# Performance work log

Hardware: AMD Instinct MI355X
Metric: run time of the kernel (lower is better)

## Reference

```python
import jax, jax.numpy as jnp
import numpy as np


def setup_inputs() -> dict:
    key = jax.random.key(0)
    k1, k2, k3, k4 = jax.random.split(key, 4)
    N, E, D_IN, D_OUT = 100000, 1600000, 128, 128
    x = jax.random.normal(k1, (N, D_IN), dtype=jnp.float32)
    # nn.Linear weight has shape [out_channels, in_channels]
    weight = jax.random.normal(k2, (D_OUT, D_IN), dtype=jnp.float32) * (1.0 / np.sqrt(D_IN))
    # COO sparse A_hat: row 0 = dst (i), row 1 = src (j)
    edge_index = jax.random.randint(k3, (2, E), 0, N, dtype=jnp.int64)
    edge_vals = jax.random.uniform(k4, (E,), dtype=jnp.float32)
    return {
        "x": x,
        "weight": weight,
        "edge_index": edge_index,
        "edge_vals": edge_vals,
        "num_nodes": N,
    }


def reference(x, weight, edge_index, edge_vals, num_nodes):
    # H = x @ W^T  (nn.Linear without bias)
    h = jnp.einsum("ni,oi->no", x, weight)  # [N, out]
    dst = edge_index[0]
    src = edge_index[1]
    # sparse A_hat @ H: out[i] = sum over edges (i<-j) of a_ij * h[j]
    msgs = edge_vals[:, None] * h[src]  # [E, out]
    out = jax.ops.segment_sum(msgs, dst, num_segments=num_nodes)
    return out
```

## Files before the change

### kernel.cpp

```cpp
#include <hip/hip_runtime.h>

#define D 128
#define SCAN_BLK 1024
#define BM 64
#define BM2 128
#define KC 32
#define BSH 6
#define BNODES 64

using short8 = __attribute__((ext_vector_type(8))) short;
using floatx4 = __attribute__((ext_vector_type(4))) float;

__device__ __forceinline__ unsigned int f2bf(unsigned int b) {
    return (b + 0x7fffu + ((b >> 16) & 1u)) >> 16;
}

__global__ void transpose_w_kernel(const float* __restrict__ w, float* __restrict__ wt) {
    int t = blockIdx.x * 256 + threadIdx.x;
    if (t < D * D) {
        int o = t >> 7;
        int k = t & 127;
        wt[k * D + o] = w[t];
    }
}

__global__ void prep_wbfs_kernel(const float* __restrict__ w, unsigned short* __restrict__ wbfs) {
    int t = blockIdx.x * 256 + threadIdx.x;
    if (t < D * D) {
        int n = t >> 7, k = t & 127;
        wbfs[n * 128 + (k ^ ((n & 7) << 3))] = (unsigned short)f2bf(__float_as_uint(w[t]));
    }
}

__global__ __launch_bounds__(256) void x_to_bf16_kernel(const float* __restrict__ x,
                                                        unsigned int* __restrict__ xbf,
                                                        long long nvec) {
    long long i = (long long)blockIdx.x * 256 + threadIdx.x;
    long long stride = (long long)gridDim.x * 256;
    for (; i < nvec; i += stride) {
        float4 v = ((const float4*)x)[i];
        unsigned int b0 = f2bf(__float_as_uint(v.x)), b1 = f2bf(__float_as_uint(v.y));
        unsigned int b2 = f2bf(__float_as_uint(v.z)), b3 = f2bf(__float_as_uint(v.w));
        ((uint2*)xbf)[i] = make_uint2(b0 | (b1 << 16), b2 | (b3 << 16));
    }
}

__global__ __launch_bounds__(512) void bhist_kernel(const int* __restrict__ ei, int* bhist,
                                                    int E, int NB) {
    __shared__ int h[2048];
    int tid = threadIdx.x;
    for (int i = tid; i < NB; i += 512) h[i] = 0;
    __syncthreads();
    for (long long e = (long long)blockIdx.x * 512 + tid; e < E; e += (long long)gridDim.x * 512)
        atomicAdd(&h[((unsigned)ei[e]) >> BSH], 1);
    __syncthreads();
    for (int i = tid; i < NB; i += 512)
        if (h[i]) atomicAdd(&bhist[i], h[i]);
}

__global__ __launch_bounds__(SCAN_BLK) void scan_blocks_kernel(const int* __restrict__ deg,
                                                               int* inscan, int* blksum, int n) {
    __shared__ int s[SCAN_BLK];
    int gid = blockIdx.x * SCAN_BLK + threadIdx.x;
    int v = (gid < n) ? deg[gid] : 0;
    s[threadIdx.x] = v;
    __syncthreads();
    for (int d = 1; d < SCAN_BLK; d <<= 1) {
        int t = (threadIdx.x >= d) ? s[threadIdx.x - d] : 0;
        __syncthreads();
        s[threadIdx.x] += t;
        __syncthreads();
    }
    if (gid < n) inscan[gid] = s[threadIdx.x];
    if (threadIdx.x == SCAN_BLK - 1) blksum[blockIdx.x] = s[SCAN_BLK - 1];
}

__global__ __launch_bounds__(128) void scan_sums_kernel(const int* __restrict__ blksum,
                                                        int* blkoff, int nblk) {
    __shared__ int s[128];
    int v = (threadIdx.x < nblk) ? blksum[threadIdx.x] : 0;
    s[threadIdx.x] = v;
    __syncthreads();
    for (int d = 1; d < 128; d <<= 1) {
        int t = (threadIdx.x >= d) ? s[threadIdx.x - d] : 0;
        __syncthreads();
        s[threadIdx.x] += t;
        __syncthreads();
    }
    if (threadIdx.x < nblk) blkoff[threadIdx.x] = s[threadIdx.x] - v;
}

__global__ void bucket_finalize_kernel(const int* __restrict__ bhist,
                                       const int* __restrict__ binscan,
                                       const int* __restrict__ bblkoff,
                                       int* bbase, int* bcursor, int* off,
                                       int NB, int N, int E) {
    int g = blockIdx.x * 256 + threadIdx.x;
    if (g < NB) {
        int o = bblkoff[g >> 10] + binscan[g] - bhist[g];
        bbase[g] = o;
        bcursor[g] = o;
    }
    if (g == 0) { bbase[NB] = E; off[N] = E; }
}

__global__ __launch_bounds__(512) void binA_kernel(const int* __restrict__ ei,
                                                   const float* __restrict__ ev,
                                                   int* bcursor, int2* __restrict__ ebin,
                                                   int E, int NB) {
    __shared__ int hist[2048];
    __shared__ int base[2048];
    __shared__ int cnt2[2048];
    int tid = threadIdx.x;
    for (int i = tid; i < NB; i += 512) { hist[i] = 0; cnt2[i] = 0; }
    __syncthreads();
    int e0 = blockIdx.x * 8192;
#pragma unroll
    for (int i = 0; i < 16; ++i) {
        int e = e0 + i * 512 + tid;
        if (e < E) atomicAdd(&hist[((unsigned)ei[e]) >> BSH], 1);
    }
    __syncthreads();
    for (int i = tid; i < NB; i += 512)
        if (hist[i]) base[i] = atomicAdd(&bcursor[i], hist[i]);
    __syncthreads();
#pragma unroll
    for (int i = 0; i < 16; ++i) {
        int e = e0 + i * 512 + tid;
        if (e < E) {
            int dst = ei[e];
            int b = ((unsigned)dst) >> BSH;
            int pos = base[b] + atomicAdd(&cnt2[b], 1);
            ebin[pos] = make_int2(ei[E + e] | ((dst & (BNODES - 1)) << 26),
                                  __float_as_int(ev[e]));
        }
    }
}

__global__ __launch_bounds__(512) void binB2_kernel(const int* __restrict__ bbase,
                                                    const int2* __restrict__ ebin,
                                                    int* __restrict__ off,
                                                    int2* __restrict__ srt, int N) {
    __shared__ int degL[BNODES];
    __shared__ int cum[BNODES];
    __shared__ int cnt2[BNODES];
    int b = blockIdx.x;
    int tid = threadIdx.x;
    if (tid < BNODES) { degL[tid] = 0; cnt2[tid] = 0; }
    __syncthreads();
    int start = bbase[b], end = bbase[b + 1];
    for (int p = start + tid; p < end; p += 512)
        atomicAdd(&degL[((unsigned)ebin[p].x) >> 26], 1);
    __syncthreads();
    if (tid == 0) {
        int run = start;
#pragma unroll
        for (int i = 0; i < BNODES; ++i) { cum[i] = run; run += degL[i]; }
    }
    __syncthreads();
    int node0 = b << BSH;
    if (tid < BNODES && node0 + tid < N) off[node0 + tid] = cum[tid];
    for (int p = start + tid; p < end; p += 512) {
        int2 eb = ebin[p];
        int dl = ((unsigned)eb.x) >> 26;
        int pos = cum[dl] + atomicAdd(&cnt2[dl], 1);
        srt[pos] = make_int2(eb.x & 0x03FFFFFF, eb.y);
    }
}

__global__ void hist_rank_kernel(const int* __restrict__ ei, int* deg,
                                 unsigned short* __restrict__ rank, int E) {
    int e = blockIdx.x * 256 + threadIdx.x;
    if (e < E) rank[e] = (unsigned short)atomicAdd(&deg[ei[e]], 1);
}

__global__ void finalize_offsets_kernel(const int* __restrict__ deg,
                                        const int* __restrict__ inscan,
                                        const int* __restrict__ blkoff,
                                        int* off, int n, int E) {
    int gid = blockIdx.x * 256 + threadIdx.x;
    if (gid < n) off[gid] = blkoff[gid >> 10] + inscan[gid] - deg[gid];
    if (gid == 0) off[n] = E;
}

__global__ void edge_scatter2_kernel(const int* __restrict__ ei, const float* __restrict__ ev,
                                     const int* __restrict__ off,
                                     const unsigned short* __restrict__ rank,
                                     int2* __restrict__ srt, int E) {
    int e = blockIdx.x * 256 + threadIdx.x;
    if (e < E) {
        int dst = ei[e];
        int pos = off[dst] + (int)rank[e];
        srt[pos] = make_int2(ei[E + e], __float_as_int(ev[e]));
    }
}

template <bool AGGBF>
__global__ __launch_bounds__(256) void gather_bf16_kernel(const int* __restrict__ off,
                                                          const int2* __restrict__ srt,
                                                          const unsigned int* __restrict__ xbf,
                                                          float* __restrict__ out,
                                                          unsigned int* __restrict__ aggbf,
                                                          int N) {
    int lane = threadIdx.x & 63;
    int wid = blockIdx.x * 4 + (threadIdx.x >> 6);
    if (wid >= N) return;
    int beg = off[wid], end = off[wid + 1];
    float2 acc = make_float2(0.f, 0.f);
    int e = beg;
    for (; e + 3 < end; e += 4) {
        int2 s0 = srt[e], s1 = srt[e + 1], s2 = srt[e + 2], s3 = srt[e + 3];
        unsigned int u0 = xbf[(size_t)s0.x * 64 + lane];
        unsigned int u1 = xbf[(size_t)s1.x * 64 + lane];
        unsigned int u2 = xbf[(size_t)s2.x * 64 + lane];
        unsigned int u3 = xbf[(size_t)s3.x * 64 + lane];
        float v0 = __int_as_float(s0.y), v1 = __int_as_float(s1.y);
        float v2 = __int_as_float(s2.y), v3 = __int_as_float(s3.y);
        acc.x = fmaf(v0, __uint_as_float(u0 << 16), acc.x);
        acc.y = fmaf(v0, __uint_as_float(u0 & 0xffff0000u), acc.y);
        acc.x = fmaf(v1, __uint_as_float(u1 << 16), acc.x);
        acc.y = fmaf(v1, __uint_as_float(u1 & 0xffff0000u), acc.y);
        acc.x = fmaf(v2, __uint_as_float(u2 << 16), acc.x);
        acc.y = fmaf(v2, __uint_as_float(u2 & 0xffff0000u), acc.y);
        acc.x = fmaf(v3, __uint_as_float(u3 << 16), acc.x);
        acc.y = fmaf(v3, __uint_as_float(u3 & 0xffff0000u), acc.y);
    }
    for (; e < end; ++e) {
        int2 sv = srt[e];
        unsigned int u = xbf[(size_t)sv.x * 64 + lane];
        float v = __int_as_float(sv.y);
        acc.x = fmaf(v, __uint_as_float(u << 16), acc.x);
        acc.y = fmaf(v, __uint_as_float(u & 0xffff0000u), acc.y);
    }
    if (AGGBF) {
        unsigned int pk = f2bf(__float_as_uint(acc.x)) | (f2bf(__float_as_uint(acc.y)) << 16);
        aggbf[(size_t)wid * 64 + lane] = pk;
    } else {
        *(float2*)&out[(size_t)wid * D + lane * 2] = acc;
    }
}

__global__ __launch_bounds__(512) void linear_mfma_bf2_kernel(const unsigned int* __restrict__ aggbf,
                                                              const unsigned short* __restrict__ wbfs,
                                                              float* __restrict__ out, int N) {
    __shared__ __align__(16) unsigned short sW[D * D];
    __shared__ __align__(16) unsigned short sA[BM2 * D];
    int t = threadIdx.x;
    int row0 = blockIdx.x * BM2;
    {
        const uint4* src = (const uint4*)wbfs;
        uint4* dst = (uint4*)sW;
#pragma unroll
        for (int i = 0; i < 4; ++i) dst[i * 512 + t] = src[i * 512 + t];
    }
#pragma unroll
    for (int it = 0; it < 4; ++it) {
        int iv = it * 512 + t;
        int m = iv >> 4;
        int q = iv & 15;
        int r = row0 + m;
        int rcl = r < N ? r : N - 1;
        uint4 v = *(const uint4*)&aggbf[(size_t)rcl * 64 + q * 4];
        *(uint4*)((char*)sA + m * 256 + ((q * 16) ^ ((m & 7) << 4))) = v;
    }
    __syncthreads();

    int lane = t & 63;
    int w = t >> 6;
    int lm = 16 * w + (lane & 15);
    int ln = lane & 15;
    int kg = lane >> 4;

    floatx4 acc[8];
#pragma unroll
    for (int nt = 0; nt < 8; ++nt) acc[nt] = (floatx4){0.f, 0.f, 0.f, 0.f};

#pragma unroll
    for (int ks = 0; ks < 4; ++ks) {
        int kbyte = ks * 64 + kg * 16;
        short8 a = *(const short8*)((const char*)sA + lm * 256 + (kbyte ^ ((lm & 7) << 4)));
#pragma unroll
        for (int nt = 0; nt < 8; ++nt) {
            int n = nt * 16 + ln;
            short8 bfr = *(const short8*)((const char*)sW + n * 256 + (kbyte ^ ((n & 7) << 4)));
            acc[nt] = __builtin_amdgcn_mfma_f32_16x16x32_bf16(a, bfr, acc[nt], 0, 0, 0);
        }
    }

    int rbase = row0 + 16 * w + 4 * kg;
#pragma unroll
    for (int nt = 0; nt < 8; ++nt) {
#pragma unroll
        for (int r = 0; r < 4; ++r) {
            int row = rbase + r;
            if (row < N) out[(size_t)row * D + nt * 16 + ln] = acc[nt][r];
        }
    }
}

__global__ __launch_bounds__(256) void linear_mfma_kernel(float* io,
                                                          const unsigned short* __restrict__ wbfs,
                                                          int N) {
    __shared__ __align__(16) unsigned short sW[D * D];
    __shared__ __align__(16) unsigned short sA[BM * D];
    int t = threadIdx.x;
    int row0 = blockIdx.x * BM;
    {
        const uint4* src = (const uint4*)wbfs;
        uint4* dst = (uint4*)sW;
#pragma unroll
        for (int i = 0; i < 8; ++i) dst[i * 256 + t] = src[i * 256 + t];
    }
#pragma unroll
    for (int it = 0; it < 8; ++it) {
        int idx = it * 1024 + t * 4;
        int m = idx >> 7;
        int k0 = idx & 127;
        int r = row0 + m;
        int rcl = r < N ? r : N - 1;
        float4 v = *(const float4*)&io[(size_t)rcl * D + k0];
        unsigned int b0 = f2bf(__float_as_uint(v.x)), b1 = f2bf(__float_as_uint(v.y));
        unsigned int b2 = f2bf(__float_as_uint(v.z)), b3 = f2bf(__float_as_uint(v.w));
        int byteoff = m * 256 + ((k0 * 2) ^ ((m & 7) << 4));
        *(uint2*)((char*)sA + byteoff) = make_uint2(b0 | (b1 << 16), b2 | (b3 << 16));
    }
    __syncthreads();

    int lane = t & 63;
    int w = t >> 6;
    int lm = 16 * w + (lane & 15);
    int ln = lane & 15;
    int kg = lane >> 4;

    floatx4 acc[8];
#pragma unroll
    for (int nt = 0; nt < 8; ++nt) acc[nt] = (floatx4){0.f, 0.f, 0.f, 0.f};

#pragma unroll
    for (int ks = 0; ks < 4; ++ks) {
        int kbyte = ks * 64 + kg * 16;
        short8 a = *(const short8*)((const char*)sA + lm * 256 + (kbyte ^ ((lm & 7) << 4)));
#pragma unroll
        for (int nt = 0; nt < 8; ++nt) {
            int n = nt * 16 + ln;
            short8 bfr = *(const short8*)((const char*)sW + n * 256 + (kbyte ^ ((n & 7) << 4)));
            acc[nt] = __builtin_amdgcn_mfma_f32_16x16x32_bf16(a, bfr, acc[nt], 0, 0, 0);
        }
    }

    int rbase = row0 + 16 * w + 4 * kg;
#pragma unroll
    for (int nt = 0; nt < 8; ++nt) {
#pragma unroll
        for (int r = 0; r < 4; ++r) {
            int row = rbase + r;
            if (row < N) io[(size_t)row * D + nt * 16 + ln] = acc[nt][r];
        }
    }
}

__global__ __launch_bounds__(256) void scatter_kernel(const int* __restrict__ ei,
                                                      const float* __restrict__ ev,
                                                      const float* __restrict__ x,
                                                      float* agg, int E) {
    int lane = threadIdx.x & 63;
    long long wid = (long long)blockIdx.x * 4 + (threadIdx.x >> 6);
    long long nw = (long long)gridDim.x * 4;
    for (long long e = wid; e < E; e += nw) {
        int i = ei[e];
        int j = ei[(long long)E + e];
        float v = ev[e];
        float2 xv = *(const float2*)&x[(size_t)j * D + lane * 2];
        float* op = &agg[(size_t)i * D + lane * 2];
        unsafeAtomicAdd(&op[0], v * xv.x);
        unsafeAtomicAdd(&op[1], v * xv.y);
    }
}

__global__ __launch_bounds__(256) void linear_tiled_kernel(float* io,
                                                           const float* __restrict__ wt,
                                                           int N) {
    __shared__ float sA[KC][BM + 4];
    __shared__ float sW2[KC][D];
    int t = threadIdx.x;
    int tc = t & 15;
    int tr = t >> 4;
    int row0 = blockIdx.x * BM;

    float acc[4][8];
#pragma unroll
    for (int i = 0; i < 4; ++i)
#pragma unroll
        for (int j = 0; j < 8; ++j) acc[i][j] = 0.f;

    int ldA_r = t >> 3;
    int ldA_k = (t & 7) * 4;
    int ldW_k = t >> 5;
    int ldW_c = (t & 31) * 4;

    for (int kc = 0; kc < D; kc += KC) {
#pragma unroll
        for (int rr = 0; rr < BM; rr += 32) {
            int r = row0 + ldA_r + rr;
            int rcl = r < N ? r : N - 1;
            float4 v = *(const float4*)&io[(size_t)rcl * D + kc + ldA_k];
            sA[ldA_k + 0][ldA_r + rr] = v.x;
            sA[ldA_k + 1][ldA_r + rr] = v.y;
            sA[ldA_k + 2][ldA_r + rr] = v.z;
            sA[ldA_k + 3][ldA_r + rr] = v.w;
        }
#pragma unroll
        for (int kk = 0; kk < KC; kk += 8)
            *(float4*)&sW2[ldW_k + kk][ldW_c] =
                *(const float4*)&wt[(size_t)(kc + ldW_k + kk) * D + ldW_c];
        __syncthreads();

#pragma unroll 8
        for (int k = 0; k < KC; ++k) {
            float4 a = *(const float4*)&sA[k][tr * 4];
            float4 w0 = *(const float4*)&sW2[k][tc * 8];
            float4 w1 = *(const float4*)&sW2[k][tc * 8 + 4];
            float av[4] = {a.x, a.y, a.z, a.w};
            float wv[8] = {w0.x, w0.y, w0.z, w0.w, w1.x, w1.y, w1.z, w1.w};
#pragma unroll
            for (int i = 0; i < 4; ++i)
#pragma unroll
                for (int j = 0; j < 8; ++j)
                    acc[i][j] = fmaf(av[i], wv[j], acc[i][j]);
        }
        __syncthreads();
    }

#pragma unroll
    for (int i = 0; i < 4; ++i) {
        int r = row0 + tr * 4 + i;
        if (r < N) {
            *(float4*)&io[(size_t)r * D + tc * 8] = *(float4*)&acc[i][0];
            *(float4*)&io[(size_t)r * D + tc * 8 + 4] = *(float4*)&acc[i][4];
        }
    }
}

extern "C" void kernel_launch(void* const* d_in, const int* in_sizes, int n_in,
                              void* d_out, int out_size, void* d_ws, size_t ws_size,
                              hipStream_t stream) {
    const float* x = (const float*)d_in[0];
    const float* w = (const float*)d_in[1];
    const int* ei = (const int*)d_in[2];
    const float* ev = (const float*)d_in[3];

    int N = in_sizes[0] / D;
    int E = in_sizes[3];
    int nblk = (N + SCAN_BLK - 1) / SCAN_BLK;
    int NB = (N + BNODES - 1) >> BSH;
    int nblkB = (NB + SCAN_BLK - 1) / SCAN_BLK;

    float* out = (float*)d_out;

    char* p = (char*)d_ws;
    float* wt = (float*)p;            p += (size_t)D * D * sizeof(float);
    unsigned short* wbfs = (unsigned short*)p;  p += (size_t)D * D * sizeof(unsigned short);
    int* deg = (int*)p;               p += (size_t)N * sizeof(int);
    int* inscan = (int*)p;            p += (size_t)N * sizeof(int);
    int* off = (int*)p;               p += (size_t)(N + 1) * sizeof(int);
    int* blksum = (int*)p;            p += (size_t)nblk * sizeof(int);
    int* blkoff = (int*)p;            p += (size_t)nblk * sizeof(int);
    p = (char*)(((uintptr_t)p + 255) & ~(uintptr_t)255);
    int* bhist = (int*)p;             p += (size_t)NB * sizeof(int);
    int* binscan = (int*)p;           p += (size_t)NB * sizeof(int);
    int* bbase = (int*)p;             p += (size_t)(NB + 1) * sizeof(int);
    int* bcursor = (int*)p;           p += (size_t)NB * sizeof(int);
    int* bblksum = (int*)p;           p += (size_t)(nblkB + 1) * sizeof(int);
    int* bblkoff = (int*)p;           p += (size_t)(nblkB + 1) * sizeof(int);
    p = (char*)(((uintptr_t)p + 255) & ~(uintptr_t)255);
    unsigned short* rank = (unsigned short*)p;  p += (size_t)E * sizeof(unsigned short);
    p = (char*)(((uintptr_t)p + 255) & ~(uintptr_t)255);
    int2* srt = (int2*)p;             p += (size_t)E * sizeof(int2);
    size_t needed_t2 = (size_t)(p - (char*)d_ws);
    p = (char*)(((uintptr_t)p + 255) & ~(uintptr_t)255);
    unsigned int* xbf = (unsigned int*)p;  p += (size_t)N * (D / 2) * sizeof(unsigned int);
    size_t needed_t1 = (size_t)(p - (char*)d_ws);
    p = (char*)(((uintptr_t)p + 255) & ~(uintptr_t)255);
    size_t ebin_bytes = (size_t)E * sizeof(int2);
    size_t aggbf_bytes = (size_t)N * (D / 2) * sizeof(unsigned int);
    int2* ebin = (int2*)p;
    unsigned int* aggbf = (unsigned int*)p;
    p += (ebin_bytes > aggbf_bytes ? ebin_bytes : aggbf_bytes);
    size_t needed_t0 = (size_t)(p - (char*)d_ws);

    if (ws_size >= needed_t0 && N < (1 << 26) && NB <= 2048) {
        prep_wbfs_kernel<<<(D * D + 255) / 256, 256, 0, stream>>>(w, wbfs);
        hipMemsetAsync(bhist, 0, (size_t)NB * sizeof(int), stream);
        x_to_bf16_kernel<<<2048, 256, 0, stream>>>(x, xbf, (long long)N * D / 4);
        bhist_kernel<<<200, 512, 0, stream>>>(ei, bhist, E, NB);
        scan_blocks_kernel<<<nblkB, SCAN_BLK, 0, stream>>>(bhist, binscan, bblksum, NB);
        scan_sums_kernel<<<1, 128, 0, stream>>>(bblksum, bblkoff, nblkB);
        bucket_finalize_kernel<<<(NB + 255) / 256, 256, 0, stream>>>(
            bhist, binscan, bblkoff, bbase, bcursor, off, NB, N, E);
        binA_kernel<<<(E + 8191) / 8192, 512, 0, stream>>>(ei, ev, bcursor, ebin, E, NB);
        binB2_kernel<<<NB, 512, 0, stream>>>(bbase, ebin, off, srt, N);
        gather_bf16_kernel<true><<<(N + 3) / 4, 256, 0, stream>>>(off, srt, xbf, out, aggbf, N);
        linear_mfma_bf2_kernel<<<(N + BM2 - 1) / BM2, 512, 0, stream>>>(aggbf, wbfs, out, N);
    } else if (ws_size >= needed_t1) {
        prep_wbfs_kernel<<<(D * D + 255) / 256, 256, 0, stream>>>(w, wbfs);
        hipMemsetAsync(deg, 0, (size_t)N * sizeof(int), stream);
        x_to_bf16_kernel<<<2048, 256, 0, stream>>>(x, xbf, (long long)N * D / 4);
        hist_rank_kernel<<<(E + 255) / 256, 256, 0, stream>>>(ei, deg, rank, E);
        scan_blocks_kernel<<<nblk, SCAN_BLK, 0, stream>>>(deg, inscan, blksum, N);
        scan_sums_kernel<<<1, 128, 0, stream>>>(blksum, blkoff, nblk);
        finalize_offsets_kernel<<<(N + 255) / 256, 256, 0, stream>>>(deg, inscan, blkoff,
                                                                     off, N, E);
        edge_scatter2_kernel<<<(E + 255) / 256, 256, 0, stream>>>(ei, ev, off, rank, srt, E);
        gather_bf16_kernel<false><<<(N + 3) / 4, 256, 0, stream>>>(off, srt, xbf, out,
                                                                   aggbf, N);
        linear_mfma_kernel<<<(N + BM - 1) / BM, 256, 0, stream>>>(out, wbfs, N);
    } else {
        transpose_w_kernel<<<(D * D + 255) / 256, 256, 0, stream>>>(w, wt);
        hipMemsetAsync(d_out, 0, (size_t)out_size * sizeof(float), stream);
        scatter_kernel<<<4096, 256, 0, stream>>>(ei, ev, x, out, E);
        linear_tiled_kernel<<<(N + BM - 1) / BM, 256, 0, stream>>>(out, wt, N);
    }
}
```

Before: 169.2 us.

## Fuse preprocessing launches and unroll gather loop to 8 edges

Cuts the launch count of the bucketed path. The bhist memset moves into prep_wbfs, the bf16 conversion of x and the bucket histogram are combined into one kernel by partitioning blocks between the two jobs, and the three-kernel bucket scan becomes a single 1024-thread block scan. The gather kernel now reads 8 edges per iteration using 64-bit nontemporal loads, which puts more independent loads in flight. The costs are more register pressure and a single-block scan that only handles NB up to 2048.

```diff
diff --git a/kernel.cpp b/kernel.cpp
--- a/kernel.cpp
+++ b/kernel.cpp
@@ -24,11 +24,187 @@
     }
 }
 
-__global__ void prep_wbfs_kernel(const float* __restrict__ w, unsigned short* __restrict__ wbfs) {
+__global__ void prep_wbfs_kernel(const float* __restrict__ w, unsigned short* __restrict__ wbfs,
+                                 int* bhist, int NB) {
     int t = blockIdx.x * 256 + threadIdx.x;
     if (t < D * D) {
         int n = t >> 7, k = t & 127;
         wbfs[n * 128 + (k ^ ((n & 7) << 3))] = (unsigned short)f2bf(__float_as_uint(w[t]));
+    }
+    for (int i = t; i < NB; i += gridDim.x * 256) bhist[i] = 0;
+}
+
+__global__ __launch_bounds__(256) void x2bf_bhist_kernel(const float* __restrict__ x,
+                                                         unsigned int* __restrict__ xbf,
+                                                         long long nvec,
+                                                         const int* __restrict__ ei,
+                                                         int* bhist, int E, int NB, int xb) {
+    __shared__ int h[2048];
+    if ((int)blockIdx.x < xb) {
+        long long i = (long long)blockIdx.x * 256 + threadIdx.x;
+        long long stride = (long long)xb * 256;
+        for (; i < nvec; i += stride) {
+            float4 v = ((const float4*)x)[i];
+            unsigned int b0 = f2bf(__float_as_uint(v.x)), b1 = f2bf(__float_as_uint(v.y));
+            unsigned int b2 = f2bf(__float_as_uint(v.z)), b3 = f2bf(__float_as_uint(v.w));
+            ((uint2*)xbf)[i] = make_uint2(b0 | (b1 << 16), b2 | (b3 << 16));
+        }
+    } else {
+        int tid = threadIdx.x;
+        for (int i = tid; i < NB; i += 256) h[i] = 0;
+        __syncthreads();
+        int hb = blockIdx.x - xb;
+        int nhb = gridDim.x - xb;
+        for (long long e = (long long)hb * 256 + tid; e < E; e += (long long)nhb * 256)
+            atomicAdd(&h[((unsigned)ei[e]) >> BSH], 1);
+        __syncthreads();
+        for (int i = tid; i < NB; i += 256)
+            if (h[i]) atomicAdd(&bhist[i], h[i]);
+    }
+}
+
+__global__ __launch_bounds__(1024) void bucket_scan_kernel(const int* __restrict__ bhist,
+                                                           int* bbase, int* bcursor, int* off,
+                                                           int NB, int N, int E) {
+    __shared__ int s[1024];
+    int t = threadIdx.x;
+    int a = (2 * t < NB) ? bhist[2 * t] : 0;
+    int b = (2 * t + 1 < NB) ? bhist[2 * t + 1] : 0;
+    int sum = a + b;
+    s[t] = sum;
+    __syncthreads();
+    for (int d = 1; d < 1024; d <<= 1) {
+        int v = (t >= d) ? s[t - d] : 0;
+        __syncthreads();
+        s[t] += v;
+        __syncthreads();
+    }
+    int excl = s[t] - sum;
+    if (2 * t < NB) { bbase[2 * t] = excl; bcursor[2 * t] = excl; }
+    if (2 * t + 1 < NB) { bbase[2 * t + 1] = excl + a; bcursor[2 * t + 1] = excl + a; }
+    if (t == 0) { bbase[NB] = E; off[N] = E; }
+}
+
+__global__ __launch_bounds__(512) void binA_kernel(const int* __restrict__ ei,
+                                                   const float* __restrict__ ev,
+                                                   int* bcursor, int2* __restrict__ ebin,
+                                                   int E, int NB) {
+    __shared__ int hist[2048];
+    __shared__ int base[2048];
+    __shared__ int cnt2[2048];
+    int tid = threadIdx.x;
+    for (int i = tid; i < NB; i += 512) { hist[i] = 0; cnt2[i] = 0; }
+    __syncthreads();
+    int e0 = blockIdx.x * 8192;
+#pragma unroll
+    for (int i = 0; i < 16; ++i) {
+        int e = e0 + i * 512 + tid;
+        if (e < E) atomicAdd(&hist[((unsigned)ei[e]) >> BSH], 1);
+    }
+    __syncthreads();
+    for (int i = tid; i < NB; i += 512)
+        if (hist[i]) base[i] = atomicAdd(&bcursor[i], hist[i]);
+    __syncthreads();
+#pragma unroll
+    for (int i = 0; i < 16; ++i) {
+        int e = e0 + i * 512 + tid;
+        if (e < E) {
+            int dst = ei[e];
+            int b = ((unsigned)dst) >> BSH;
+            int pos = base[b] + atomicAdd(&cnt2[b], 1);
+            ebin[pos] = make_int2(ei[E + e] | ((dst & (BNODES - 1)) << 26),
+                                  __float_as_int(ev[e]));
+        }
+    }
+}
+
+__global__ __launch_bounds__(512) void binB2_kernel(const int* __restrict__ bbase,
+                                                    const int2* __restrict__ ebin,
+                                                    int* __restrict__ off,
+                                                    int2* __restrict__ srt, int N) {
+    __shared__ int degL[BNODES];
+    __shared__ int cum[BNODES];
+    __shared__ int cnt2[BNODES];
+    int b = blockIdx.x;
+    int tid = threadIdx.x;
+    if (tid < BNODES) { degL[tid] = 0; cnt2[tid] = 0; }
+    __syncthreads();
+    int start = bbase[b], end = bbase[b + 1];
+    for (int p = start + tid; p < end; p += 512)
+        atomicAdd(&degL[((unsigned)ebin[p].x) >> 26], 1);
+    __syncthreads();
+    if (tid == 0) {
+        int run = start;
+#pragma unroll
+        for (int i = 0; i < BNODES; ++i) { cum[i] = run; run += degL[i]; }
+    }
+    __syncthreads();
+    int node0 = b << BSH;
+    if (tid < BNODES && node0 + tid < N) off[node0 + tid] = cum[tid];
+    for (int p = start + tid; p < end; p += 512) {
+        int2 eb = ebin[p];
+        int dl = ((unsigned)eb.x) >> 26;
+        int pos = cum[dl] + atomicAdd(&cnt2[dl], 1);
+        srt[pos] = make_int2(eb.x & 0x03FFFFFF, eb.y);
+    }
+}
+
+__global__ void hist_rank_kernel(const int* __restrict__ ei, int* deg,
+                                 unsigned short* __restrict__ rank, int E) {
+    int e = blockIdx.x * 256 + threadIdx.x;
+    if (e < E) rank[e] = (unsigned short)atomicAdd(&deg[ei[e]], 1);
+}
+
+__global__ __launch_bounds__(SCAN_BLK) void scan_blocks_kernel(const int* __restrict__ deg,
+                                                               int* inscan, int* blksum, int n) {
+    __shared__ int s[SCAN_BLK];
+    int gid = blockIdx.x * SCAN_BLK + threadIdx.x;
+    int v = (gid < n) ? deg[gid] : 0;
+    s[threadIdx.x] = v;
+    __syncthreads();
+    for (int d = 1; d < SCAN_BLK; d <<= 1) {
+        int t = (threadIdx.x >= d) ? s[threadIdx.x - d] : 0;
+        __syncthreads();
+        s[threadIdx.x] += t;
+        __syncthreads();
+    }
+    if (gid < n) inscan[gid] = s[threadIdx.x];
+    if (threadIdx.x == SCAN_BLK - 1) blksum[blockIdx.x] = s[SCAN_BLK - 1];
+}
+
+__global__ __launch_bounds__(128) void scan_sums_kernel(const int* __restrict__ blksum,
+                                                        int* blkoff, int nblk) {
+    __shared__ int s[128];
+    int v = (threadIdx.x < nblk) ? blksum[threadIdx.x] : 0;
+    s[threadIdx.x] = v;
+    __syncthreads();
+    for (int d = 1; d < 128; d <<= 1) {
+        int t = (threadIdx.x >= d) ? s[threadIdx.x - d] : 0;
+        __syncthreads();
+        s[threadIdx.x] += t;
+        __syncthreads();
+    }
+    if (threadIdx.x < nblk) blkoff[threadIdx.x] = s[threadIdx.x] - v;
+}
+
+__global__ void finalize_offsets_kernel(const int* __restrict__ deg,
+                                        const int* __restrict__ inscan,
+                                        const int* __restrict__ blkoff,
+                                        int* off, int n, int E) {
+    int gid = blockIdx.x * 256 + threadIdx.x;
+    if (gid < n) off[gid] = blkoff[gid >> 10] + inscan[gid] - deg[gid];
+    if (gid == 0) off[n] = E;
+}
+
+__global__ void edge_scatter2_kernel(const int* __restrict__ ei, const float* __restrict__ ev,
+                                     const int* __restrict__ off,
+                                     const unsigned short* __restrict__ rank,
+                                     int2* __restrict__ srt, int E) {
+    int e = blockIdx.x * 256 + threadIdx.x;
+    if (e < E) {
+        int dst = ei[e];
+        int pos = off[dst] + (int)rank[e];
+        srt[pos] = make_int2(ei[E + e], __float_as_int(ev[e]));
     }
 }
 
@@ -42,156 +218,6 @@
         unsigned int b0 = f2bf(__float_as_uint(v.x)), b1 = f2bf(__float_as_uint(v.y));
         unsigned int b2 = f2bf(__float_as_uint(v.z)), b3 = f2bf(__float_as_uint(v.w));
         ((uint2*)xbf)[i] = make_uint2(b0 | (b1 << 16), b2 | (b3 << 16));
-    }
-}
-
-__global__ __launch_bounds__(512) void bhist_kernel(const int* __restrict__ ei, int* bhist,
-                                                    int E, int NB) {
-    __shared__ int h[2048];
-    int tid = threadIdx.x;
-    for (int i = tid; i < NB; i += 512) h[i] = 0;
-    __syncthreads();
-    for (long long e = (long long)blockIdx.x * 512 + tid; e < E; e += (long long)gridDim.x * 512)
-        atomicAdd(&h[((unsigned)ei[e]) >> BSH], 1);
-    __syncthreads();
-    for (int i = tid; i < NB; i += 512)
-        if (h[i]) atomicAdd(&bhist[i], h[i]);
-}
-
-__global__ __launch_bounds__(SCAN_BLK) void scan_blocks_kernel(const int* __restrict__ deg,
-                                                               int* inscan, int* blksum, int n) {
-    __shared__ int s[SCAN_BLK];
-    int gid = blockIdx.x * SCAN_BLK + threadIdx.x;
-    int v = (gid < n) ? deg[gid] : 0;
-    s[threadIdx.x] = v;
-    __syncthreads();
-    for (int d = 1; d < SCAN_BLK; d <<= 1) {
-        int t = (threadIdx.x >= d) ? s[threadIdx.x - d] : 0;
-        __syncthreads();
-        s[threadIdx.x] += t;
-        __syncthreads();
-    }
-    if (gid < n) inscan[gid] = s[threadIdx.x];
-    if (threadIdx.x == SCAN_BLK - 1) blksum[blockIdx.x] = s[SCAN_BLK - 1];
-}
-
-__global__ __launch_bounds__(128) void scan_sums_kernel(const int* __restrict__ blksum,
-                                                        int* blkoff, int nblk) {
-    __shared__ int s[128];
-    int v = (threadIdx.x < nblk) ? blksum[threadIdx.x] : 0;
-    s[threadIdx.x] = v;
-    __syncthreads();
-    for (int d = 1; d < 128; d <<= 1) {
-        int t = (threadIdx.x >= d) ? s[threadIdx.x - d] : 0;
-        __syncthreads();
-        s[threadIdx.x] += t;
-        __syncthreads();
-    }
-    if (threadIdx.x < nblk) blkoff[threadIdx.x] = s[threadIdx.x] - v;
-}
-
-__global__ void bucket_finalize_kernel(const int* __restrict__ bhist,
-                                       const int* __restrict__ binscan,
-                                       const int* __restrict__ bblkoff,
-                                       int* bbase, int* bcursor, int* off,
-                                       int NB, int N, int E) {
-    int g = blockIdx.x * 256 + threadIdx.x;
-    if (g < NB) {
-        int o = bblkoff[g >> 10] + binscan[g] - bhist[g];
-        bbase[g] = o;
-        bcursor[g] = o;
-    }
-    if (g == 0) { bbase[NB] = E; off[N] = E; }
-}
-
-__global__ __launch_bounds__(512) void binA_kernel(const int* __restrict__ ei,
-                                                   const float* __restrict__ ev,
-                                                   int* bcursor, int2* __restrict__ ebin,
-                                                   int E, int NB) {
-    __shared__ int hist[2048];
-    __shared__ int base[2048];
-    __shared__ int cnt2[2048];
-    int tid = threadIdx.x;
-    for (int i = tid; i < NB; i += 512) { hist[i] = 0; cnt2[i] = 0; }
-    __syncthreads();
-    int e0 = blockIdx.x * 8192;
-#pragma unroll
-    for (int i = 0; i < 16; ++i) {
-        int e = e0 + i * 512 + tid;
-        if (e < E) atomicAdd(&hist[((unsigned)ei[e]) >> BSH], 1);
-    }
-    __syncthreads();
-    for (int i = tid; i < NB; i += 512)
-        if (hist[i]) base[i] = atomicAdd(&bcursor[i], hist[i]);
-    __syncthreads();
-#pragma unroll
-    for (int i = 0; i < 16; ++i) {
-        int e = e0 + i * 512 + tid;
-        if (e < E) {
-            int dst = ei[e];
-            int b = ((unsigned)dst) >> BSH;
-            int pos = base[b] + atomicAdd(&cnt2[b], 1);
-            ebin[pos] = make_int2(ei[E + e] | ((dst & (BNODES - 1)) << 26),
-                                  __float_as_int(ev[e]));
-        }
-    }
-}
-
-__global__ __launch_bounds__(512) void binB2_kernel(const int* __restrict__ bbase,
-                                                    const int2* __restrict__ ebin,
-                                                    int* __restrict__ off,
-                                                    int2* __restrict__ srt, int N) {
-    __shared__ int degL[BNODES];
-    __shared__ int cum[BNODES];
-    __shared__ int cnt2[BNODES];
-    int b = blockIdx.x;
-    int tid = threadIdx.x;
-    if (tid < BNODES) { degL[tid] = 0; cnt2[tid] = 0; }
-    __syncthreads();
-    int start = bbase[b], end = bbase[b + 1];
-    for (int p = start + tid; p < end; p += 512)
-        atomicAdd(&degL[((unsigned)ebin[p].x) >> 26], 1);
-    __syncthreads();
-    if (tid == 0) {
-        int run = start;
-#pragma unroll
-        for (int i = 0; i < BNODES; ++i) { cum[i] = run; run += degL[i]; }
-    }
-    __syncthreads();
-    int node0 = b << BSH;
-    if (tid < BNODES && node0 + tid < N) off[node0 + tid] = cum[tid];
-    for (int p = start + tid; p < end; p += 512) {
-        int2 eb = ebin[p];
-        int dl = ((unsigned)eb.x) >> 26;
-        int pos = cum[dl] + atomicAdd(&cnt2[dl], 1);
-        srt[pos] = make_int2(eb.x & 0x03FFFFFF, eb.y);
-    }
-}
-
-__global__ void hist_rank_kernel(const int* __restrict__ ei, int* deg,
-                                 unsigned short* __restrict__ rank, int E) {
-    int e = blockIdx.x * 256 + threadIdx.x;
-    if (e < E) rank[e] = (unsigned short)atomicAdd(&deg[ei[e]], 1);
-}
-
-__global__ void finalize_offsets_kernel(const int* __restrict__ deg,
-                                        const int* __restrict__ inscan,
-                                        const int* __restrict__ blkoff,
-                                        int* off, int n, int E) {
-    int gid = blockIdx.x * 256 + threadIdx.x;
-    if (gid < n) off[gid] = blkoff[gid >> 10] + inscan[gid] - deg[gid];
-    if (gid == 0) off[n] = E;
-}
-
-__global__ void edge_scatter2_kernel(const int* __restrict__ ei, const float* __restrict__ ev,
-                                     const int* __restrict__ off,
-                                     const unsigned short* __restrict__ rank,
-                                     int2* __restrict__ srt, int E) {
-    int e = blockIdx.x * 256 + threadIdx.x;
-    if (e < E) {
-        int dst = ei[e];
-        int pos = off[dst] + (int)rank[e];
-        srt[pos] = make_int2(ei[E + e], __float_as_int(ev[e]));
     }
 }
 
@@ -208,27 +234,41 @@
     int beg = off[wid], end = off[wid + 1];
     float2 acc = make_float2(0.f, 0.f);
     int e = beg;
+    const unsigned long long* srt8 = (const unsigned long long*)srt;
+    for (; e + 7 < end; e += 8) {
+        unsigned long long q[8];
+        unsigned int u[8];
+#pragma unroll
+        for (int j = 0; j < 8; ++j) q[j] = __builtin_nontemporal_load(&srt8[e + j]);
+#pragma unroll
+        for (int j = 0; j < 8; ++j)
+            u[j] = xbf[(size_t)(unsigned int)q[j] * 64 + lane];
+#pragma unroll
+        for (int j = 0; j < 8; ++j) {
+            float v = __uint_as_float((unsigned int)(q[j] >> 32));
+            acc.x = fmaf(v, __uint_as_float(u[j] << 16), acc.x);
+            acc.y = fmaf(v, __uint_as_float(u[j] & 0xffff0000u), acc.y);
+        }
+    }
     for (; e + 3 < end; e += 4) {
-        int2 s0 = srt[e], s1 = srt[e + 1], s2 = srt[e + 2], s3 = srt[e + 3];
-        unsigned int u0 = xbf[(size_t)s0.x * 64 + lane];
-        unsigned int u1 = xbf[(size_t)s1.x * 64 + lane];
-        unsigned int u2 = xbf[(size_t)s2.x * 64 + lane];
-        unsigned int u3 = xbf[(size_t)s3.x * 64 + lane];
-        float v0 = __int_as_float(s0.y), v1 = __int_as_float(s1.y);
-        float v2 = __int_as_float(s2.y), v3 = __int_as_float(s3.y);
-        acc.x = fmaf(v0, __uint_as_float(u0 << 16), acc.x);
-        acc.y = fmaf(v0, __uint_as_float(u0 & 0xffff0000u), acc.y);
-        acc.x = fmaf(v1, __uint_as_float(u1 << 16), acc.x);
-        acc.y = fmaf(v1, __uint_as_float(u1 & 0xffff0000u), acc.y);
-        acc.x = fmaf(v2, __uint_as_float(u2 << 16), acc.x);
-        acc.y = fmaf(v2, __uint_as_float(u2 & 0xffff0000u), acc.y);
-        acc.x = fmaf(v3, __uint_as_float(u3 << 16), acc.x);
-        acc.y = fmaf(v3, __uint_as_float(u3 & 0xffff0000u), acc.y);
+        unsigned long long q[4];
+        unsigned int u[4];
+#pragma unroll
+        for (int j = 0; j < 4; ++j) q[j] = __builtin_nontemporal_load(&srt8[e + j]);
+#pragma unroll
+        for (int j = 0; j < 4; ++j)
+            u[j] = xbf[(size_t)(unsigned int)q[j] * 64 + lane];
+#pragma unroll
+        for (int j = 0; j < 4; ++j) {
+            float v = __uint_as_float((unsigned int)(q[j] >> 32));
+            acc.x = fmaf(v, __uint_as_float(u[j] << 16), acc.x);
+            acc.y = fmaf(v, __uint_as_float(u[j] & 0xffff0000u), acc.y);
+        }
     }
     for (; e < end; ++e) {
-        int2 sv = srt[e];
-        unsigned int u = xbf[(size_t)sv.x * 64 + lane];
-        float v = __int_as_float(sv.y);
+        unsigned long long q = __builtin_nontemporal_load(&srt8[e]);
+        unsigned int u = xbf[(size_t)(unsigned int)q * 64 + lane];
+        float v = __uint_as_float((unsigned int)(q >> 32));
         acc.x = fmaf(v, __uint_as_float(u << 16), acc.x);
         acc.y = fmaf(v, __uint_as_float(u & 0xffff0000u), acc.y);
     }
@@ -453,7 +493,6 @@
     int E = in_sizes[3];
     int nblk = (N + SCAN_BLK - 1) / SCAN_BLK;
     int NB = (N + BNODES - 1) >> BSH;
-    int nblkB = (NB + SCAN_BLK - 1) / SCAN_BLK;
 
     float* out = (float*)d_out;
 
@@ -467,11 +506,8 @@
     int* blkoff = (int*)p;            p += (size_t)nblk * sizeof(int);
     p = (char*)(((uintptr_t)p + 255) & ~(uintptr_t)255);
     int* bhist = (int*)p;             p += (size_t)NB * sizeof(int);
-    int* binscan = (int*)p;           p += (size_t)NB * sizeof(int);
     int* bbase = (int*)p;             p += (size_t)(NB + 1) * sizeof(int);
     int* bcursor = (int*)p;           p += (size_t)NB * sizeof(int);
-    int* bblksum = (int*)p;           p += (size_t)(nblkB + 1) * sizeof(int);
-    int* bblkoff = (int*)p;           p += (size_t)(nblkB + 1) * sizeof(int);
     p = (char*)(((uintptr_t)p + 255) & ~(uintptr_t)255);
     unsigned short* rank = (unsigned short*)p;  p += (size_t)E * sizeof(unsigned short);
     p = (char*)(((uintptr_t)p + 255) & ~(uintptr_t)255);
@@ -489,20 +525,17 @@
     size_t needed_t0 = (size_t)(p - (char*)d_ws);
 
     if (ws_size >= needed_t0 && N < (1 << 26) && NB <= 2048) {
-        prep_wbfs_kernel<<<(D * D + 255) / 256, 256, 0, stream>>>(w, wbfs);
-        hipMemsetAsync(bhist, 0, (size_t)NB * sizeof(int), stream);
-        x_to_bf16_kernel<<<2048, 256, 0, stream>>>(x, xbf, (long long)N * D / 4);
-        bhist_kernel<<<200, 512, 0, stream>>>(ei, bhist, E, NB);
-        scan_blocks_kernel<<<nblkB, SCAN_BLK, 0, stream>>>(bhist, binscan, bblksum, NB);
-        scan_sums_kernel<<<1, 128, 0, stream>>>(bblksum, bblkoff, nblkB);
-        bucket_finalize_kernel<<<(NB + 255) / 256, 256, 0, stream>>>(
-            bhist, binscan, bblkoff, bbase, bcursor, off, NB, N, E);
+        const int xb = 1024, hb = 512;
+        prep_wbfs_kernel<<<(D * D + 255) / 256, 256, 0, stream>>>(w, wbfs, bhist, NB);
+        x2bf_bhist_kernel<<<xb + hb, 256, 0, stream>>>(x, xbf, (long long)N * D / 4,
+                                                       ei, bhist, E, NB, xb);
+        bucket_scan_kernel<<<1, 1024, 0, stream>>>(bhist, bbase, bcursor, off, NB, N, E);
         binA_kernel<<<(E + 8191) / 8192, 512, 0, stream>>>(ei, ev, bcursor, ebin, E, NB);
         binB2_kernel<<<NB, 512, 0, stream>>>(bbase, ebin, off, srt, N);
         gather_bf16_kernel<true><<<(N + 3) / 4, 256, 0, stream>>>(off, srt, xbf, out, aggbf, N);
         linear_mfma_bf2_kernel<<<(N + BM2 - 1) / BM2, 512, 0, stream>>>(aggbf, wbfs, out, N);
     } else if (ws_size >= needed_t1) {
-        prep_wbfs_kernel<<<(D * D + 255) / 256, 256, 0, stream>>>(w, wbfs);
+        prep_wbfs_kernel<<<(D * D + 255) / 256, 256, 0, stream>>>(w, wbfs, bhist, NB);
         hipMemsetAsync(deg, 0, (size_t)N * sizeof(int), stream);
         x_to_bf16_kernel<<<2048, 256, 0, stream>>>(x, xbf, (long long)N * D / 4);
         hist_rank_kernel<<<(E + 255) / 256, 256, 0, stream>>>(ei, deg, rank, E);
```

Result: faster. 163.7 us (-3.2%).
